# Kernel tuning notes

Hardware: AMD Instinct MI355X
Metric: run time of the kernel (lower is better)

## Reference

```python
import jax, jax.numpy as jnp
import numpy as np

OMEGA = 32  # recall threshold from init_kwargs


def setup_inputs() -> dict:
    key = jax.random.key(0)
    B, T, F, H = 32, 1024, 256, 256
    stdv = 1.0 / np.sqrt(H).astype(np.float32)
    ks = jax.random.split(key, 10)
    u = lambda k, shape: jax.random.uniform(k, shape, jnp.float32, -stdv, stdv)
    return {
        "x": jax.random.normal(ks[0], (B, T, F), jnp.float32),
        "W": u(ks[1], (F, 4 * H)),
        "U": u(ks[2], (H, 4 * H)),
        "P": u(ks[3], (B, 2 * B)),
        "B_bias": u(ks[4], (4 * H,)),
        "W_r": u(ks[5], (F, 1)),
        "P_r": u(ks[6], (1, B)),
        "U_r": u(ks[7], (H, 1)),
        "W_out": u(ks[8], (H, 1)),
        "b_out": u(ks[9], (1,)),
    }


def reference(x, W, U, P, B_bias, W_r, P_r, U_r, W_out, b_out):
    Bsz, T, F = x.shape
    H = U.shape[0]
    xs = jnp.swapaxes(x, 0, 1)  # [T, B, F]
    h0 = jnp.zeros((Bsz, H), x.dtype)
    c0 = jnp.zeros((Bsz, H), x.dtype)
    Xm0 = jnp.zeros((T, Bsz, F), x.dtype)  # states_array: stored x_t per step
    Hm0 = jnp.zeros((T, Bsz, H), x.dtype)  # states_array: stored h_t per step

    def step(carry, inp):
        h, c, Xm, Hm = carry
        x_t, t = inp  # x_t: [B, F], t: scalar int (== len(states_array) before append)
        # recall gate: sigmoid(P_r @ (x_t @ W_r + h @ U_r)) -> [1,1]
        gate = jax.nn.sigmoid(P_r @ (x_t @ W_r + h @ U_r))[0, 0]
        # best index = round(t * gate); clip to valid range (source would IndexError at t)
        idx = jnp.clip(jnp.round(t.astype(x.dtype) * gate).astype(jnp.int32), 0, jnp.maximum(t - 1, 0))
        use_self = t < OMEGA
        x_rec = jnp.where(use_self, x_t, Xm[idx])
        h_rec = jnp.where(use_self, h, Hm[idx])
        # append current (x_t, h_t) to the memory bank
        Xm = Xm.at[t].set(x_t)
        Hm = Hm.at[t].set(h)
        # x_t_prime = [x_t; x_rec] (2B rows); fold the vstack into a concat of the two affine maps
        a_cur = x_t @ W + h @ U      # [B, 4H]
        a_rec = x_rec @ W + h_rec @ U  # [B, 4H]
        gates = P @ jnp.concatenate([a_cur, a_rec], axis=0) + B_bias  # [B, 4H]
        i_t, f_t, g_t, _o_raw = jnp.split(gates, 4, axis=1)
        i_t = jax.nn.sigmoid(i_t)
        f_t = jax.nn.sigmoid(f_t)
        g_t = jnp.tanh(g_t)
        o_t = i_t  # faithful to source: o_t = sigmoid(i chunk), not the o chunk
        c = f_t * c + i_t * g_t
        h = o_t * jnp.tanh(c)
        return (h, c, Xm, Hm), None

    (h, c, _, _), _ = jax.lax.scan(step, (h0, c0, Xm0, Hm0), (xs, jnp.arange(T)))
    return h @ W_out + b_out  # [B, 1]
```

## Files before the change

### kernel.cpp

```cpp
#include <hip/hip_runtime.h>
#include <cstdint>
#include <cstddef>


#define T_STEPS 1024
#define BSZ 32
#define FDIM 256
#define HDIM 256
#define G3W 384
#define KWG 64
#define HS 4
#define JC 12
#define HPAD 260
#define OMEGA 32
#define HSLICE 8192

static const size_t AXC_BYTES = (size_t)KWG * T_STEPS * G3W * sizeof(float);
static const size_t HB_BYTES  = (size_t)(T_STEPS + 1) * HSLICE * sizeof(float);
static const size_t GX_BYTES  = (size_t)T_STEPS * sizeof(double);

__global__ __launch_bounds__(256) void phaseA(const float* __restrict__ x,
                                              const float* __restrict__ W,
                                              const float* __restrict__ W_r,
                                              const float* __restrict__ P_r,
                                              float* __restrict__ AXc,
                                              double* __restrict__ gx) {
  const int t = blockIdx.x;
  const int tid = threadIdx.x;
  __shared__ __align__(16) float xs[BSZ][HPAD];
  __shared__ double sred[BSZ];

  for (int i = tid; i < BSZ * FDIM / 4; i += 256) {
    const int b = (i * 4) >> 8;
    const int k = (i * 4) & 255;
    *(float4*)&xs[b][k] = *(const float4*)&x[((size_t)b * T_STEPS + t) * FDIM + k];
  }
  __syncthreads();

  for (int pass = 0; pass < 3; ++pass) {
    const int j = pass * 256 + tid;
    float acc[BSZ];
#pragma unroll
    for (int b = 0; b < BSZ; ++b) acc[b] = 0.f;
    for (int k0 = 0; k0 < FDIM; k0 += 4) {
      const float w0 = W[(size_t)(k0 + 0) * 1024 + j];
      const float w1 = W[(size_t)(k0 + 1) * 1024 + j];
      const float w2 = W[(size_t)(k0 + 2) * 1024 + j];
      const float w3 = W[(size_t)(k0 + 3) * 1024 + j];
#pragma unroll
      for (int b = 0; b < BSZ; ++b) {
        const float4 xv = *(const float4*)&xs[b][k0];
        acc[b] = fmaf(xv.x, w0, acc[b]);
        acc[b] = fmaf(xv.y, w1, acc[b]);
        acc[b] = fmaf(xv.z, w2, acc[b]);
        acc[b] = fmaf(xv.w, w3, acc[b]);
      }
    }
    const int wgj = (j >> 2) & 63;
    const int slot = ((j >> 8) << 2) | (j & 3);
    float* dst = AXc + ((size_t)wgj * T_STEPS + t) * G3W + slot;
    for (int b = 0; b < BSZ; ++b) dst[b * 12] = acc[b];
  }

  if (tid < BSZ) {
    double s = 0.0;
    for (int k = 0; k < FDIM; k += 4) {
      const float4 xv = *(const float4*)&xs[tid][k];
      const float4 wv = *(const float4*)&W_r[k];
      s = fma((double)xv.x, (double)wv.x, s);
      s = fma((double)xv.y, (double)wv.y, s);
      s = fma((double)xv.z, (double)wv.z, s);
      s = fma((double)xv.w, (double)wv.w, s);
    }
    sred[tid] = s;
  }
  __syncthreads();
  if (tid == 0) {
    double g = 0.0;
    for (int b = 0; b < BSZ; ++b) g = fma((double)P_r[b], sred[b], g);
    gx[t] = g;
  }
}

__global__ __launch_bounds__(256) void phaseB(const float* __restrict__ U,
                                              const float* __restrict__ P,
                                              const float* __restrict__ B_bias,
                                              const float* __restrict__ P_r,
                                              const float* __restrict__ U_r,
                                              float* __restrict__ AXc,
                                              float* __restrict__ hbank,
                                              const double* __restrict__ gx,
                                              unsigned int* __restrict__ cnt) {
  const int wg = blockIdx.x;
  const int tid = threadIdx.x;
  const int lane = tid & 63;

  __shared__ __align__(16) float ULt[JC][HPAD];
  __shared__ __align__(16) float hL[BSZ][HPAD];
  __shared__ __align__(16) float PL[BSZ][64];
  __shared__ __align__(16) float acs[JC][36];
  __shared__ __align__(16) float ars[JC][36];
  __shared__ __align__(16) float red1[BSZ][JC];
  __shared__ __align__(16) float UrL[FDIM];
  __shared__ float PrL[BSZ];
  __shared__ float biasL[JC];

  for (int i = tid; i < JC * HDIM; i += 256) {
    const int jc = i >> 8, k = i & 255;
    const int col = (jc >> 2) * HDIM + wg * HS + (jc & 3);
    ULt[jc][k] = U[(size_t)k * 1024 + col];
  }
  for (int i = tid; i < BSZ * 64; i += 256) PL[i >> 6][i & 63] = P[i];
  if (tid < FDIM) UrL[tid] = U_r[tid];
  if (tid < BSZ) PrL[tid] = P_r[tid];
  if (tid < JC) biasL[tid] = B_bias[(tid >> 2) * HDIM + wg * HS + (tid & 3)];

  const int u = (tid >= 64) ? (tid - 64) : 0;
  const int khalf = u / 96;
  const int rmap = u % 96;
  const int jcp = rmap % 6, bA = rmap / 6;
  const int jc0 = 2 * jcp, jc1 = jc0 + 1;
  const int bB = bA + 16;
  const int kb = khalf * 128;

  const int ob = tid >> 2, ohc = tid & 3;
  const int grow = tid & 31;
  const int gc0 = (tid >> 5) * 4;

  float* __restrict__ AXwg = AXc + (size_t)wg * T_STEPS * G3W;

  float creg = 0.f;
  __syncthreads();

  for (int t = 0; t < T_STEPS; ++t) {
    float2 xwA = {0.f, 0.f}, xwB = {0.f, 0.f};
    size_t aA = 0, aB = 0;
    if (tid >= 64 && tid < 160) {
      aA = (size_t)t * G3W + bA * JC + jc0;
      aB = (size_t)t * G3W + bB * JC + jc0;
      xwA = *(const float2*)&AXwg[aA];
      xwB = *(const float2*)&AXwg[aB];
    }
    double gxt = 0.0;
    if (tid == 0) gxt = gx[t];

    if (t > 0) {
      if (tid < 64) {
        const unsigned tgt = 8u * (unsigned)t;
        int guard = 0;
        for (;;) {
          unsigned v = tgt;
          if (lane < 8) {
            v = __hip_atomic_load(&cnt[lane * 32], __ATOMIC_RELAXED,
                                  __HIP_MEMORY_SCOPE_AGENT);
          }
          if (__all((int)(v >= tgt))) break;
          if (++guard > (1 << 20)) break;
        }
      }
      __syncthreads();
      asm volatile("" ::: "memory");
    }

    {
      const uint64_t base =
          (uint64_t)(hbank + (size_t)t * HSLICE) + (uint64_t)tid * 16u;
      const uint64_t a0 = base;
      const uint64_t a1 = base + 4096u;
      const uint64_t a2 = base + 8192u;
      const uint64_t a3 = base + 12288u;
      const uint64_t a4 = base + 16384u;
      const uint64_t a5 = base + 20480u;
      const uint64_t a6 = base + 24576u;
      const uint64_t a7 = base + 28672u;
      float4 r0, r1, r2, r3, r4, r5, r6, r7;
      asm volatile(
          "global_load_dwordx4 %0, %8, off sc0 sc1\n\t"
          "global_load_dwordx4 %1, %9, off sc0 sc1\n\t"
          "global_load_dwordx4 %2, %10, off sc0 sc1\n\t"
          "global_load_dwordx4 %3, %11, off sc0 sc1\n\t"
          "global_load_dwordx4 %4, %12, off sc0 sc1\n\t"
          "global_load_dwordx4 %5, %13, off sc0 sc1\n\t"
          "global_load_dwordx4 %6, %14, off sc0 sc1\n\t"
          "global_load_dwordx4 %7, %15, off sc0 sc1\n\t"
          "s_waitcnt vmcnt(0)"
          : "=&v"(r0), "=&v"(r1), "=&v"(r2), "=&v"(r3),
            "=&v"(r4), "=&v"(r5), "=&v"(r6), "=&v"(r7)
          : "v"(a0), "v"(a1), "v"(a2), "v"(a3),
            "v"(a4), "v"(a5), "v"(a6), "v"(a7)
          : "memory");
      *(float4*)&hL[grow][gc0 + 0]   = r0;
      *(float4*)&hL[grow][gc0 + 32]  = r1;
      *(float4*)&hL[grow][gc0 + 64]  = r2;
      *(float4*)&hL[grow][gc0 + 96]  = r3;
      *(float4*)&hL[grow][gc0 + 128] = r4;
      *(float4*)&hL[grow][gc0 + 160] = r5;
      *(float4*)&hL[grow][gc0 + 192] = r6;
      *(float4*)&hL[grow][gc0 + 224] = r7;
    }
    __syncthreads();

    float s00 = 0.f, s01 = 0.f, s10 = 0.f, s11 = 0.f;
    if (tid < 64) {
      if (t >= OMEGA) {
        const int gb = tid & 31, kp = tid >> 5;
        double s = 0.0;
        const int k0 = kp * 128;
        for (int k = k0; k < k0 + 128; k += 4) {
          const float4 hv = *(const float4*)&hL[gb][k];
          const float4 uv = *(const float4*)&UrL[k];
          s = fma((double)hv.x, (double)uv.x, s);
          s = fma((double)hv.y, (double)uv.y, s);
          s = fma((double)hv.z, (double)uv.z, s);
          s = fma((double)hv.w, (double)uv.w, s);
        }
        s += __shfl_xor(s, 32, 64);
        double v = (double)PrL[gb] * s;
        v += __shfl_xor(v, 16, 64);
        v += __shfl_xor(v, 8, 64);
        v += __shfl_xor(v, 4, 64);
        v += __shfl_xor(v, 2, 64);
        v += __shfl_xor(v, 1, 64);
        int idx = 0;
        if (tid == 0) {
          const double g = gxt + v;
          const double gate = 1.0 / (1.0 + exp(-g));
          idx = (int)rint((double)t * gate);
          if (idx > t - 1) idx = t - 1;
          if (idx < 0) idx = 0;
        }
        idx = __shfl(idx, 0, 64);
        const float* __restrict__ src = AXwg + (size_t)idx * G3W;
        float av[6];
#pragma unroll
        for (int j = 0; j < 6; ++j) av[j] = src[lane + j * 64];
#pragma unroll
        for (int j = 0; j < 6; ++j) {
          const int f = lane + j * 64;
          ars[f % JC][f / JC] = av[j];
        }
      }
    } else {
      for (int k = kb; k < kb + 128; k += 4) {
        const float4 u0 = *(const float4*)&ULt[jc0][k];
        const float4 u1 = *(const float4*)&ULt[jc1][k];
        const float4 h0 = *(const float4*)&hL[bA][k];
        const float4 h1 = *(const float4*)&hL[bB][k];
        s00 = fmaf(h0.x, u0.x, s00); s00 = fmaf(h0.y, u0.y, s00);
        s00 = fmaf(h0.z, u0.z, s00); s00 = fmaf(h0.w, u0.w, s00);
        s01 = fmaf(h0.x, u1.x, s01); s01 = fmaf(h0.y, u1.y, s01);
        s01 = fmaf(h0.z, u1.z, s01); s01 = fmaf(h0.w, u1.w, s01);
        s10 = fmaf(h1.x, u0.x, s10); s10 = fmaf(h1.y, u0.y, s10);
        s10 = fmaf(h1.z, u0.z, s10); s10 = fmaf(h1.w, u0.w, s10);
        s11 = fmaf(h1.x, u1.x, s11); s11 = fmaf(h1.y, u1.y, s11);
        s11 = fmaf(h1.z, u1.z, s11); s11 = fmaf(h1.w, u1.w, s11);
      }
      if (khalf == 1) {
        *(float2*)&red1[bA][jc0] = make_float2(s00, s01);
        *(float2*)&red1[bB][jc0] = make_float2(s10, s11);
      }
    }
    __syncthreads();

    if (tid >= 64 && tid < 160) {
      const float2 rA = *(const float2*)&red1[bA][jc0];
      const float2 rB = *(const float2*)&red1[bB][jc0];
      const float v00 = s00 + rA.x + xwA.x;
      const float v01 = s01 + rA.y + xwA.y;
      const float v10 = s10 + rB.x + xwB.x;
      const float v11 = s11 + rB.y + xwB.y;
      *(float2*)&AXwg[aA] = make_float2(v00, v01);
      *(float2*)&AXwg[aB] = make_float2(v10, v11);
      acs[jc0][bA] = v00;  acs[jc1][bA] = v01;
      acs[jc0][bB] = v10;  acs[jc1][bB] = v11;
      if (t < OMEGA) {
        ars[jc0][bA] = v00;  ars[jc1][bA] = v01;
        ars[jc0][bB] = v10;  ars[jc1][bB] = v11;
      }
    }
    __syncthreads();

    if (tid < BSZ * HS) {
      float gi = biasL[ohc];
      float gf = biasL[4 + ohc];
      float gg = biasL[8 + ohc];
#pragma unroll
      for (int b4 = 0; b4 < BSZ; b4 += 4) {
        const float4 pv = *(const float4*)&PL[ob][b4];
        const float4 ai = *(const float4*)&acs[ohc][b4];
        const float4 af = *(const float4*)&acs[4 + ohc][b4];
        const float4 ag = *(const float4*)&acs[8 + ohc][b4];
        gi = fmaf(pv.x, ai.x, gi); gi = fmaf(pv.y, ai.y, gi);
        gi = fmaf(pv.z, ai.z, gi); gi = fmaf(pv.w, ai.w, gi);
        gf = fmaf(pv.x, af.x, gf); gf = fmaf(pv.y, af.y, gf);
        gf = fmaf(pv.z, af.z, gf); gf = fmaf(pv.w, af.w, gf);
        gg = fmaf(pv.x, ag.x, gg); gg = fmaf(pv.y, ag.y, gg);
        gg = fmaf(pv.z, ag.z, gg); gg = fmaf(pv.w, ag.w, gg);
      }
#pragma unroll
      for (int b4 = 0; b4 < BSZ; b4 += 4) {
        const float4 pv = *(const float4*)&PL[ob][BSZ + b4];
        const float4 ai = *(const float4*)&ars[ohc][b4];
        const float4 af = *(const float4*)&ars[4 + ohc][b4];
        const float4 ag = *(const float4*)&ars[8 + ohc][b4];
        gi = fmaf(pv.x, ai.x, gi); gi = fmaf(pv.y, ai.y, gi);
        gi = fmaf(pv.z, ai.z, gi); gi = fmaf(pv.w, ai.w, gi);
        gf = fmaf(pv.x, af.x, gf); gf = fmaf(pv.y, af.y, gf);
        gf = fmaf(pv.z, af.z, gf); gf = fmaf(pv.w, af.w, gf);
        gg = fmaf(pv.x, ag.x, gg); gg = fmaf(pv.y, ag.y, gg);
        gg = fmaf(pv.z, ag.z, gg); gg = fmaf(pv.w, ag.w, gg);
      }
      const float iv = 1.f / (1.f + expf(-gi));
      const float fv = 1.f / (1.f + expf(-gf));
      const float gv = tanhf(gg);
      creg = fmaf(fv, creg, iv * gv);
      const float hv = iv * tanhf(creg);
      const uint64_t daddr =
          (uint64_t)(hbank + (size_t)(t + 1) * HSLICE + (size_t)wg * (BSZ * HS)) +
          (uint64_t)tid * 4u;
      asm volatile(
          "global_store_dword %0, %1, off sc0 sc1\n\t"
          "s_waitcnt vmcnt(0)"
          :: "v"(daddr), "v"(hv)
          : "memory");
    }
    __syncthreads();
    if (tid == 0) {
      __hip_atomic_fetch_add(&cnt[(wg & 7) * 32], 1u, __ATOMIC_RELAXED,
                             __HIP_MEMORY_SCOPE_AGENT);
    }
  }
}

__global__ void outK(const float* __restrict__ hbank, const float* __restrict__ W_out,
                     const float* __restrict__ b_out, float* __restrict__ out) {
  const int b = threadIdx.x;
  if (b < BSZ) {
    const float* h = hbank + (size_t)T_STEPS * HSLICE;
    float s = 0.f;
    for (int wg = 0; wg < KWG; ++wg) {
      const float4 hv = *(const float4*)&h[wg * (BSZ * HS) + b * HS];
      const float4 wv = *(const float4*)&W_out[wg * HS];
      s = fmaf(hv.x, wv.x, s); s = fmaf(hv.y, wv.y, s);
      s = fmaf(hv.z, wv.z, s); s = fmaf(hv.w, wv.w, s);
    }
    out[b] = s + b_out[0];
  }
}

extern "C" void kernel_launch(void* const* d_in, const int* in_sizes, int n_in,
                              void* d_out, int out_size, void* d_ws, size_t ws_size,
                              hipStream_t stream) {
  const float* x      = (const float*)d_in[0];
  const float* W      = (const float*)d_in[1];
  const float* U      = (const float*)d_in[2];
  const float* P      = (const float*)d_in[3];
  const float* B_bias = (const float*)d_in[4];
  const float* W_r    = (const float*)d_in[5];
  const float* P_r    = (const float*)d_in[6];
  const float* U_r    = (const float*)d_in[7];
  const float* W_out  = (const float*)d_in[8];
  const float* b_out  = (const float*)d_in[9];

  char* ws = (char*)d_ws;
  float*    AXc   = (float*)ws;
  float*    hbank = (float*)(ws + AXC_BYTES);
  double*   gx    = (double*)(ws + AXC_BYTES + HB_BYTES);
  unsigned* cnt   = (unsigned*)(ws + AXC_BYTES + HB_BYTES + GX_BYTES);

  hipMemsetAsync(hbank, 0, (size_t)HSLICE * sizeof(float), stream);
  hipMemsetAsync(cnt, 0, 1024, stream);

  phaseA<<<T_STEPS, 256, 0, stream>>>(x, W, W_r, P_r, AXc, gx);
  phaseB<<<KWG, 256, 0, stream>>>(U, P, B_bias, P_r, U_r, AXc, hbank, gx, cnt);
  outK<<<1, 64, 0, stream>>>(hbank, W_out, b_out, (float*)d_out);
}
```

Baseline: 5.260 ms.

## Replace counter barrier with sentinel-polled data flags on hidden-state bank

```diff
diff --git a/kernel.cpp b/kernel.cpp
--- a/kernel.cpp
+++ b/kernel.cpp
@@ -19,6 +19,10 @@
 static const size_t HB_BYTES  = (size_t)(T_STEPS + 1) * HSLICE * sizeof(float);
 static const size_t GX_BYTES  = (size_t)T_STEPS * sizeof(double);
 
+__device__ __forceinline__ uint32_t uminv(uint32_t a, uint32_t b) {
+  return a < b ? a : b;
+}
+
 __global__ __launch_bounds__(256) void phaseA(const float* __restrict__ x,
                                               const float* __restrict__ W,
                                               const float* __restrict__ W_r,
@@ -89,8 +93,7 @@
                                               const float* __restrict__ U_r,
                                               float* __restrict__ AXc,
                                               float* __restrict__ hbank,
-                                              const double* __restrict__ gx,
-                                              unsigned int* __restrict__ cnt) {
+                                              const double* __restrict__ gx) {
   const int wg = blockIdx.x;
   const int tid = threadIdx.x;
   const int lane = tid & 63;
@@ -143,24 +146,6 @@
     }
     double gxt = 0.0;
     if (tid == 0) gxt = gx[t];
-
-    if (t > 0) {
-      if (tid < 64) {
-        const unsigned tgt = 8u * (unsigned)t;
-        int guard = 0;
-        for (;;) {
-          unsigned v = tgt;
-          if (lane < 8) {
-            v = __hip_atomic_load(&cnt[lane * 32], __ATOMIC_RELAXED,
-                                  __HIP_MEMORY_SCOPE_AGENT);
-          }
-          if (__all((int)(v >= tgt))) break;
-          if (++guard > (1 << 20)) break;
-        }
-      }
-      __syncthreads();
-      asm volatile("" ::: "memory");
-    }
 
     {
       const uint64_t base =
@@ -174,21 +159,38 @@
       const uint64_t a6 = base + 24576u;
       const uint64_t a7 = base + 28672u;
       float4 r0, r1, r2, r3, r4, r5, r6, r7;
-      asm volatile(
-          "global_load_dwordx4 %0, %8, off sc0 sc1\n\t"
-          "global_load_dwordx4 %1, %9, off sc0 sc1\n\t"
-          "global_load_dwordx4 %2, %10, off sc0 sc1\n\t"
-          "global_load_dwordx4 %3, %11, off sc0 sc1\n\t"
-          "global_load_dwordx4 %4, %12, off sc0 sc1\n\t"
-          "global_load_dwordx4 %5, %13, off sc0 sc1\n\t"
-          "global_load_dwordx4 %6, %14, off sc0 sc1\n\t"
-          "global_load_dwordx4 %7, %15, off sc0 sc1\n\t"
-          "s_waitcnt vmcnt(0)"
-          : "=&v"(r0), "=&v"(r1), "=&v"(r2), "=&v"(r3),
-            "=&v"(r4), "=&v"(r5), "=&v"(r6), "=&v"(r7)
-          : "v"(a0), "v"(a1), "v"(a2), "v"(a3),
-            "v"(a4), "v"(a5), "v"(a6), "v"(a7)
-          : "memory");
+      int guard = 0;
+      for (;;) {
+        asm volatile(
+            "global_load_dwordx4 %0, %8, off sc0 sc1\n\t"
+            "global_load_dwordx4 %1, %9, off sc0 sc1\n\t"
+            "global_load_dwordx4 %2, %10, off sc0 sc1\n\t"
+            "global_load_dwordx4 %3, %11, off sc0 sc1\n\t"
+            "global_load_dwordx4 %4, %12, off sc0 sc1\n\t"
+            "global_load_dwordx4 %5, %13, off sc0 sc1\n\t"
+            "global_load_dwordx4 %6, %14, off sc0 sc1\n\t"
+            "global_load_dwordx4 %7, %15, off sc0 sc1\n\t"
+            "s_waitcnt vmcnt(0)"
+            : "=&v"(r0), "=&v"(r1), "=&v"(r2), "=&v"(r3),
+              "=&v"(r4), "=&v"(r5), "=&v"(r6), "=&v"(r7)
+            : "v"(a0), "v"(a1), "v"(a2), "v"(a3),
+              "v"(a4), "v"(a5), "v"(a6), "v"(a7)
+            : "memory");
+        uint32_t m = 0xFFFFFFFFu;
+#define CHK(f) m = uminv(m, ~__float_as_uint(f))
+        CHK(r0.x); CHK(r0.y); CHK(r0.z); CHK(r0.w);
+        CHK(r1.x); CHK(r1.y); CHK(r1.z); CHK(r1.w);
+        CHK(r2.x); CHK(r2.y); CHK(r2.z); CHK(r2.w);
+        CHK(r3.x); CHK(r3.y); CHK(r3.z); CHK(r3.w);
+        CHK(r4.x); CHK(r4.y); CHK(r4.z); CHK(r4.w);
+        CHK(r5.x); CHK(r5.y); CHK(r5.z); CHK(r5.w);
+        CHK(r6.x); CHK(r6.y); CHK(r6.z); CHK(r6.w);
+        CHK(r7.x); CHK(r7.y); CHK(r7.z); CHK(r7.w);
+#undef CHK
+        if (m != 0u) break;
+        if (++guard > (1 << 16)) break;
+        __builtin_amdgcn_s_sleep(1);
+      }
       *(float4*)&hL[grow][gc0 + 0]   = r0;
       *(float4*)&hL[grow][gc0 + 32]  = r1;
       *(float4*)&hL[grow][gc0 + 64]  = r2;
@@ -324,11 +326,6 @@
           :: "v"(daddr), "v"(hv)
           : "memory");
     }
-    __syncthreads();
-    if (tid == 0) {
-      __hip_atomic_fetch_add(&cnt[(wg & 7) * 32], 1u, __ATOMIC_RELAXED,
-                             __HIP_MEMORY_SCOPE_AGENT);
-    }
   }
 }
 
@@ -366,12 +363,11 @@
   float*    AXc   = (float*)ws;
   float*    hbank = (float*)(ws + AXC_BYTES);
   double*   gx    = (double*)(ws + AXC_BYTES + HB_BYTES);
-  unsigned* cnt   = (unsigned*)(ws + AXC_BYTES + HB_BYTES + GX_BYTES);
-
+
+  hipMemsetAsync(hbank, 0xFF, HB_BYTES, stream);
   hipMemsetAsync(hbank, 0, (size_t)HSLICE * sizeof(float), stream);
-  hipMemsetAsync(cnt, 0, 1024, stream);
 
   phaseA<<<T_STEPS, 256, 0, stream>>>(x, W, W_r, P_r, AXc, gx);
-  phaseB<<<KWG, 256, 0, stream>>>(U, P, B_bias, P_r, U_r, AXc, hbank, gx, cnt);
+  phaseB<<<KWG, 256, 0, stream>>>(U, P, B_bias, P_r, U_r, AXc, hbank, gx);
   outK<<<1, 64, 0, stream>>>(hbank, W_out, b_out, (float*)d_out);
 }
```

New measurement: 4.980 ms. 5.3% less time.
